# Performance work log

Measured on AMD Instinct MI355X. Metric: run time of the kernel, lower is better.

The kernel has to match this reference:

```python
import jax, jax.numpy as jnp
import numpy as np


def setup_inputs() -> dict:
    key = jax.random.key(0)
    ks = jax.random.split(key, 9)
    B, C, H, W = 1, 128, 96, 96
    Ci = C // 2
    s = 1.0 / np.sqrt(C)
    return {
        "x": jax.random.normal(ks[0], (B, C, H, W), dtype=jnp.float32),
        "theta_w": jax.random.normal(ks[1], (Ci, C), dtype=jnp.float32) * s,
        "theta_b": jax.random.normal(ks[2], (Ci,), dtype=jnp.float32) * 0.01,
        "phi_w": jax.random.normal(ks[3], (Ci, C), dtype=jnp.float32) * s,
        "phi_b": jax.random.normal(ks[4], (Ci,), dtype=jnp.float32) * 0.01,
        "g_w": jax.random.normal(ks[5], (Ci, C), dtype=jnp.float32) * s,
        "g_b": jax.random.normal(ks[6], (Ci,), dtype=jnp.float32) * 0.01,
        "out_w": jax.random.normal(ks[7], (C, Ci), dtype=jnp.float32) * (1.0 / np.sqrt(Ci)),
        "out_b": jax.random.normal(ks[8], (C,), dtype=jnp.float32) * 0.01,
    }


def reference(x, theta_w, theta_b, phi_w, phi_b, g_w, g_b, out_w, out_b):
    B, C, H, W = x.shape
    # 1x1 convs == per-position linear projections; flatten spatial to N tokens
    xf = x.transpose(0, 2, 3, 1).reshape(-1, C)          # (N, C), N = B*H*W
    theta = xf @ theta_w.T + theta_b                     # (N, Ci)
    phi = xf @ phi_w.T + phi_b                           # (N, Ci)
    g = xf @ g_w.T + g_b                                 # (N, Ci)
    # unscaled non-local attention with double softmax
    attn = jax.nn.softmax(theta @ phi.T, axis=-1)        # (N, N)
    y = jax.nn.softmax(attn @ g, axis=-1)                # (N, Ci)
    out = y @ out_w.T + out_b                            # (N, C)
    return out.reshape(B, H, W, C).transpose(0, 3, 1, 2) + x
```

## Files before the change

### kernel.cpp

```cpp
#include <hip/hip_runtime.h>
#include <hip/hip_bf16.h>

#define N_TOK 9216
#define C_IN  128
#define CI    64
#define SPLITS 8
#define L2E   1.44269504088896340736f

typedef __bf16 bf16x8 __attribute__((ext_vector_type(8)));
typedef unsigned short u16;
typedef u16 u16x4 __attribute__((ext_vector_type(4)));
typedef u16 u16x8 __attribute__((ext_vector_type(8)));
typedef unsigned u32x4 __attribute__((ext_vector_type(4)));
typedef float f32x4 __attribute__((ext_vector_type(4)));

static __device__ __forceinline__ u16 f2bf(float f) {
  return __builtin_bit_cast(u16, __float2bfloat16(f));
}
static __device__ __forceinline__ float bf2f(u16 b) {
  unsigned u = ((unsigned)b) << 16;
  return __builtin_bit_cast(float, u);
}
static __device__ __forceinline__ bf16x8 pack8(const float* f) {
  u16x8 t;
#pragma unroll
  for (int j = 0; j < 8; ++j) t[j] = f2bf(f[j]);
  return __builtin_bit_cast(bf16x8, t);
}
static __device__ __forceinline__ bf16x8 load_bf8(const u16* p) {
  u32x4 v = *(const u32x4*)p;
  return __builtin_bit_cast(bf16x8, v);
}
static __device__ __forceinline__ void gload_lds16(const void* g, void* l) {
  __builtin_amdgcn_global_load_lds(
      (const __attribute__((address_space(1))) void*)g,
      (__attribute__((address_space(3))) void*)l, 16, 0, 0);
}

#define MFMA16(a, b, c) __builtin_amdgcn_mfma_f32_16x16x32_bf16((a), (b), (c), 0, 0, 0)

__global__ __launch_bounds__(256) void k1_proj(
    const float* __restrict__ x,
    const float* __restrict__ tw, const float* __restrict__ tb,
    const float* __restrict__ pw, const float* __restrict__ pb,
    const float* __restrict__ gw, const float* __restrict__ gb,
    u16* __restrict__ thetaF, u16* __restrict__ phiF, u16* __restrict__ vF)
{
  __shared__ u16 sbuf[64 * 72];
  const int tid = threadIdx.x;
  const int w = tid >> 6, lane = tid & 63;
  const int lr = lane & 15, lg = lane >> 4;
  const int p0 = blockIdx.x * 64;
  const int m = blockIdx.y;

  bf16x8 bf[4][4];
#pragma unroll
  for (int nt = 0; nt < 4; ++nt) {
    const int p = p0 + nt * 16 + lr;
#pragma unroll
    for (int kc = 0; kc < 4; ++kc) {
      const int c0 = kc * 32 + lg * 8;
      float f[8];
#pragma unroll
      for (int j = 0; j < 8; ++j) f[j] = x[(c0 + j) * N_TOK + p];
      bf[nt][kc] = pack8(f);
    }
  }

  const float* Wm = (m == 0) ? tw : (m == 1) ? pw : gw;
  const float* Bm = (m == 0) ? tb : (m == 1) ? pb : gb;

  bf16x8 af[4];
#pragma unroll
  for (int kc = 0; kc < 4; ++kc) {
    const float* src = Wm + (w * 16 + lr) * C_IN + kc * 32 + lg * 8;
    float f[8];
#pragma unroll
    for (int j = 0; j < 8; ++j) f[j] = src[j];
    af[kc] = pack8(f);
  }
  f32x4 acc[4];
#pragma unroll
  for (int nt = 0; nt < 4; ++nt) acc[nt] = f32x4{0.f, 0.f, 0.f, 0.f};
#pragma unroll
  for (int kc = 0; kc < 4; ++kc)
#pragma unroll
    for (int nt = 0; nt < 4; ++nt)
      acc[nt] = MFMA16(af[kc], bf[nt][kc], acc[nt]);

  float bias[4];
#pragma unroll
  for (int r = 0; r < 4; ++r) bias[r] = Bm[w * 16 + lg * 4 + r];

  const float oscale = (m == 0) ? L2E : 1.0f;

  if (m < 2) {
#pragma unroll
    for (int nt = 0; nt < 4; ++nt)
#pragma unroll
      for (int r = 0; r < 4; ++r)
        sbuf[(nt * 16 + lr) * 72 + (w * 16 + lg * 4 + r)] =
            f2bf((acc[nt][r] + bias[r]) * oscale);
    __syncthreads();
    if (m == 0) {
#pragma unroll
      for (int e = 0; e < 2; ++e) {
        const int ch = tid * 2 + e;
        const int ln = ch & 63, c = (ch >> 6) & 1, qt = ch >> 7;
        const int ql = qt * 16 + (ln & 15), d = c * 32 + (ln >> 4) * 8;
        u32x4 v = *(const u32x4*)&sbuf[ql * 72 + d];
        *(u32x4*)&thetaF[(((size_t)(p0 / 16 + qt) * 2 + c) * 64 + ln) * 8] = v;
      }
    } else {
#pragma unroll
      for (int e = 0; e < 2; ++e) {
        const int ch = tid * 2 + e;
        const int ln = ch & 63, i = (ch >> 6) & 3, t = ch >> 8;
        const int kl = t * 32 + (i >> 1) * 16 + (ln & 15);
        const int d = (i & 1) * 32 + (ln >> 4) * 8;
        u32x4 v = *(const u32x4*)&sbuf[kl * 72 + d];
        *(u32x4*)&phiF[(((size_t)(p0 / 32 + t) * 4 + i) * 64 + ln) * 8] = v;
      }
    }
  } else {
#pragma unroll
    for (int nt = 0; nt < 4; ++nt)
#pragma unroll
      for (int r = 0; r < 4; ++r)
        sbuf[(w * 16 + lg * 4 + r) * 72 + nt * 16 + lr] = f2bf(acc[nt][r] + bias[r]);
    __syncthreads();
#pragma unroll
    for (int e = 0; e < 2; ++e) {
      const int ch = tid * 2 + e;
      const int ln = ch & 63, n = (ch >> 6) & 3, t = ch >> 8;
      const int d = n * 16 + (ln & 15), g4 = (ln >> 4) * 4;
      u16x4 lo = *(const u16x4*)&sbuf[d * 72 + t * 32 + g4];
      u16x4 hi = *(const u16x4*)&sbuf[d * 72 + t * 32 + 16 + g4];
      u16x8 v;
#pragma unroll
      for (int j = 0; j < 4; ++j) { v[j] = lo[j]; v[4 + j] = hi[j]; }
      *(u16x8*)&vF[(((size_t)(p0 / 32 + t) * 4 + n) * 64 + ln) * 8] = v;
    }
  }
}

__global__ __launch_bounds__(256) void k2_flash(
    const u16* __restrict__ thetaF, const u16* __restrict__ phiF,
    const u16* __restrict__ vF,
    u16* __restrict__ Opart, float* __restrict__ Lpart)
{
  __shared__ u16 kvbuf[2][8][512];
  const int tid = threadIdx.x;
  const int w = tid >> 6, lane = tid & 63;
  const int lr = lane & 15, g = lane >> 4;
  const int ks = blockIdx.x & 7;
  const int qt = blockIdx.x >> 3;
  const int q0 = qt * 128 + w * 32;
  const int NT64 = (N_TOK / SPLITS) / 64;
  const int t64base = ks * NT64;

  bf16x8 qb[2][2];
#pragma unroll
  for (int qs = 0; qs < 2; ++qs)
#pragma unroll
    for (int c = 0; c < 2; ++c)
      qb[qs][c] = load_bf8(&thetaF[(((size_t)(q0 / 16 + qs) * 2 + c) * 64 + lane) * 8]);

  f32x4 o[2][4], o4[2];
#pragma unroll
  for (int qs = 0; qs < 2; ++qs) {
#pragma unroll
    for (int n = 0; n < 4; ++n) o[qs][n] = f32x4{0.f, 0.f, 0.f, 0.f};
    o4[qs] = f32x4{0.f, 0.f, 0.f, 0.f};
  }

  u16x8 onesw;
#pragma unroll
  for (int j = 0; j < 8; ++j) onesw[j] = 0x3F80;
  const bf16x8 ones = __builtin_bit_cast(bf16x8, onesw);

  const int f0 = 2 * w;
  const size_t kgoff = (size_t)(f0 & 3) * 512 + lane * 8;
  const int hW = w >> 1;

#define STAGE(T, buf)                                                         \
  {                                                                           \
    const u16* gp = phiF + (size_t)(2 * (t64base + (T)) + hW) * 2048 + kgoff; \
    gload_lds16(gp, &kvbuf[buf][f0][0]);                                      \
    gload_lds16(gp + 512, &kvbuf[buf][f0 + 1][0]);                            \
  }

  STAGE(0, 0);
  __syncthreads();

  int cur = 0;
  for (int T = 0; T < NT64; ++T) {
    bf16x8 va[2][4];
    const u16* pV = vF + (size_t)(2 * (t64base + T)) * 2048 + lane * 8;
#pragma unroll
    for (int h = 0; h < 2; ++h)
#pragma unroll
      for (int n = 0; n < 4; ++n)
        va[h][n] = load_bf8(pV + (size_t)(h * 4 + n) * 512);

    if (T + 1 < NT64) STAGE(T + 1, cur ^ 1);

#pragma unroll
    for (int h = 0; h < 2; ++h) {
      const bf16x8 ka0 = load_bf8(&kvbuf[cur][h * 4 + 0][lane * 8]);
      const bf16x8 ka1 = load_bf8(&kvbuf[cur][h * 4 + 1][lane * 8]);
      const bf16x8 ka2 = load_bf8(&kvbuf[cur][h * 4 + 2][lane * 8]);
      const bf16x8 ka3 = load_bf8(&kvbuf[cur][h * 4 + 3][lane * 8]);

#pragma unroll
      for (int qs = 0; qs < 2; ++qs) {
        f32x4 s0 = f32x4{0.f, 0.f, 0.f, 0.f}, s1 = f32x4{0.f, 0.f, 0.f, 0.f};
        s0 = MFMA16(ka0, qb[qs][0], s0); s0 = MFMA16(ka1, qb[qs][1], s0);
        s1 = MFMA16(ka2, qb[qs][0], s1); s1 = MFMA16(ka3, qb[qs][1], s1);

        float p0v[4], p1v[4];
#pragma unroll
        for (int r = 0; r < 4; ++r) {
          p0v[r] = __builtin_amdgcn_exp2f(s0[r]);
          p1v[r] = __builtin_amdgcn_exp2f(s1[r]);
        }
        u16x8 pw;
#pragma unroll
        for (int r = 0; r < 4; ++r) { pw[r] = f2bf(p0v[r]); pw[4 + r] = f2bf(p1v[r]); }
        const bf16x8 pb = __builtin_bit_cast(bf16x8, pw);
#pragma unroll
        for (int n = 0; n < 4; ++n) o[qs][n] = MFMA16(va[h][n], pb, o[qs][n]);
        o4[qs] = MFMA16(ones, pb, o4[qs]);
      }
    }

    __syncthreads();
    cur ^= 1;
  }

  const int qg = ks * N_TOK + q0;
#pragma unroll
  for (int qs = 0; qs < 2; ++qs) {
#pragma unroll
    for (int n = 0; n < 4; ++n) {
      u16x4 ov;
#pragma unroll
      for (int r = 0; r < 4; ++r) ov[r] = f2bf(o[qs][n][r]);
      *(u16x4*)&Opart[(size_t)(qg + qs * 16 + lr) * CI + n * 16 + 4 * g] = ov;
    }
    if (lane < 16) Lpart[qg + qs * 16 + lr] = o4[qs][0];
  }
}

__global__ __launch_bounds__(256) void k2b_combine(
    const u16* __restrict__ Opart, const float* __restrict__ Lpart,
    u16* __restrict__ y)
{
  const int tid = threadIdx.x;
  const int w = tid >> 6, lane = tid & 63;
  const int q = blockIdx.x * 4 + w;

  float L = 0.f, acc = 0.f;
#pragma unroll
  for (int k = 0; k < SPLITS; ++k) {
    L += Lpart[k * N_TOK + q];
    acc += bf2f(Opart[(size_t)(k * N_TOK + q) * CI + lane]);
  }
  const float ypre = acc / L;

  float mx = ypre;
#pragma unroll
  for (int off = 1; off <= 32; off <<= 1) mx = fmaxf(mx, __shfl_xor(mx, off, 64));
  const float e = __builtin_amdgcn_exp2f((ypre - mx) * L2E);
  float s = e;
#pragma unroll
  for (int off = 1; off <= 32; off <<= 1) s += __shfl_xor(s, off, 64);
  y[q * CI + lane] = f2bf(e / s);
}

__global__ __launch_bounds__(256) void k3_out(
    const u16* __restrict__ y, const float* __restrict__ ow,
    const float* __restrict__ ob, const float* __restrict__ x,
    float* __restrict__ out)
{
  const int tid = threadIdx.x;
  const int w = tid >> 6, lane = tid & 63;
  const int lr = lane & 15, lg = lane >> 4;
  const int p0 = blockIdx.x * 32;

  bf16x8 yb[2][2];
#pragma unroll
  for (int nt = 0; nt < 2; ++nt)
#pragma unroll
    for (int kc = 0; kc < 2; ++kc)
      yb[nt][kc] = load_bf8(&y[(p0 + nt * 16 + lr) * CI + kc * 32 + lg * 8]);

#pragma unroll
  for (int mt = 0; mt < 2; ++mt) {
    bf16x8 af[2];
#pragma unroll
    for (int kc = 0; kc < 2; ++kc) {
      const float* src = ow + (w * 32 + mt * 16 + lr) * CI + kc * 32 + lg * 8;
      float f[8];
#pragma unroll
      for (int j = 0; j < 8; ++j) f[j] = src[j];
      af[kc] = pack8(f);
    }
#pragma unroll
    for (int nt = 0; nt < 2; ++nt) {
      f32x4 acc = f32x4{0.f, 0.f, 0.f, 0.f};
      acc = MFMA16(af[0], yb[nt][0], acc);
      acc = MFMA16(af[1], yb[nt][1], acc);
#pragma unroll
      for (int r = 0; r < 4; ++r) {
        const int c = w * 32 + mt * 16 + lg * 4 + r;
        const int p = p0 + nt * 16 + lr;
        out[(size_t)c * N_TOK + p] = acc[r] + ob[c] + x[(size_t)c * N_TOK + p];
      }
    }
  }
}

extern "C" void kernel_launch(void* const* d_in, const int* in_sizes, int n_in,
                              void* d_out, int out_size, void* d_ws, size_t ws_size,
                              hipStream_t stream) {
  const float* x  = (const float*)d_in[0];
  const float* tw = (const float*)d_in[1];
  const float* tb = (const float*)d_in[2];
  const float* pw = (const float*)d_in[3];
  const float* pb = (const float*)d_in[4];
  const float* gw = (const float*)d_in[5];
  const float* gb = (const float*)d_in[6];
  const float* ow = (const float*)d_in[7];
  const float* ob = (const float*)d_in[8];
  float* out = (float*)d_out;

  char* ws = (char*)d_ws;
  u16* thetaF = (u16*)(ws);
  u16* phiF   = (u16*)(ws + 1179648);
  u16* vF     = (u16*)(ws + 2 * 1179648);
  u16* yb     = (u16*)(ws + 3 * 1179648);
  u16* Op     = (u16*)(ws + 4 * 1179648);
  float* Lp   = (float*)(ws + 4 * 1179648 + 9437184);

  hipLaunchKernelGGL(k1_proj, dim3(144, 3), dim3(256), 0, stream,
                     x, tw, tb, pw, pb, gw, gb, thetaF, phiF, vF);
  hipLaunchKernelGGL(k2_flash, dim3(72 * SPLITS), dim3(256), 0, stream,
                     thetaF, phiF, vF, Op, Lp);
  hipLaunchKernelGGL(k2b_combine, dim3(N_TOK / 4), dim3(256), 0, stream,
                     Op, Lp, yb);
  hipLaunchKernelGGL(k3_out, dim3(288), dim3(256), 0, stream,
                     yb, ow, ob, x, out);
}
```

Baseline: 61.59 us.

## Stage V tiles through LDS and raise flash split count to 16

The flash kernel now stages both phi and V tiles into a double-buffered LDS buffer. All four waves issue async global-to-LDS copies, replacing the per-wave direct global loads of V, so each V tile is fetched once per block instead of once per wave. The split-K count goes from 8 to 16 when the workspace is large enough, which doubles the number of blocks for better CU occupancy. The cost is twice as many partial outputs for the combine kernel to read and reduce, plus doubled LDS use per block.

```diff
diff --git a/kernel.cpp b/kernel.cpp
--- a/kernel.cpp
+++ b/kernel.cpp
@@ -4,7 +4,6 @@
 #define N_TOK 9216
 #define C_IN  128
 #define CI    64
-#define SPLITS 8
 #define L2E   1.44269504088896340736f
 
 typedef __bf16 bf16x8 __attribute__((ext_vector_type(8)));
@@ -144,19 +143,20 @@
   }
 }
 
+template <int SPL>
 __global__ __launch_bounds__(256) void k2_flash(
     const u16* __restrict__ thetaF, const u16* __restrict__ phiF,
     const u16* __restrict__ vF,
     u16* __restrict__ Opart, float* __restrict__ Lpart)
 {
-  __shared__ u16 kvbuf[2][8][512];
+  __shared__ u16 kvbuf[2][16][512];
   const int tid = threadIdx.x;
   const int w = tid >> 6, lane = tid & 63;
   const int lr = lane & 15, g = lane >> 4;
-  const int ks = blockIdx.x & 7;
-  const int qt = blockIdx.x >> 3;
+  const int ks = blockIdx.x & (SPL - 1);
+  const int qt = blockIdx.x / SPL;
   const int q0 = qt * 128 + w * 32;
-  const int NT64 = (N_TOK / SPLITS) / 64;
+  const int NT64 = (N_TOK / SPL) / 64;
   const int t64base = ks * NT64;
 
   bf16x8 qb[2][2];
@@ -179,15 +179,18 @@
   for (int j = 0; j < 8; ++j) onesw[j] = 0x3F80;
   const bf16x8 ones = __builtin_bit_cast(bf16x8, onesw);
 
-  const int f0 = 2 * w;
-  const size_t kgoff = (size_t)(f0 & 3) * 512 + lane * 8;
-  const int hW = w >> 1;
-
-#define STAGE(T, buf)                                                         \
-  {                                                                           \
-    const u16* gp = phiF + (size_t)(2 * (t64base + (T)) + hW) * 2048 + kgoff; \
-    gload_lds16(gp, &kvbuf[buf][f0][0]);                                      \
-    gload_lds16(gp + 512, &kvbuf[buf][f0 + 1][0]);                            \
+  const u16* sbase = (w < 2) ? phiF : vF;
+  const int fbase = w * 4;
+  const int sub = w & 1;
+
+#define STAGE(T, buf)                                                          \
+  {                                                                            \
+    const u16* gp = sbase + (size_t)(2 * (t64base + (T)) + sub) * 2048 +       \
+                    lane * 8;                                                  \
+    gload_lds16(gp,        &kvbuf[buf][fbase][0]);                             \
+    gload_lds16(gp + 512,  &kvbuf[buf][fbase + 1][0]);                         \
+    gload_lds16(gp + 1024, &kvbuf[buf][fbase + 2][0]);                         \
+    gload_lds16(gp + 1536, &kvbuf[buf][fbase + 3][0]);                         \
   }
 
   STAGE(0, 0);
@@ -195,14 +198,6 @@
 
   int cur = 0;
   for (int T = 0; T < NT64; ++T) {
-    bf16x8 va[2][4];
-    const u16* pV = vF + (size_t)(2 * (t64base + T)) * 2048 + lane * 8;
-#pragma unroll
-    for (int h = 0; h < 2; ++h)
-#pragma unroll
-      for (int n = 0; n < 4; ++n)
-        va[h][n] = load_bf8(pV + (size_t)(h * 4 + n) * 512);
-
     if (T + 1 < NT64) STAGE(T + 1, cur ^ 1);
 
 #pragma unroll
@@ -211,6 +206,9 @@
       const bf16x8 ka1 = load_bf8(&kvbuf[cur][h * 4 + 1][lane * 8]);
       const bf16x8 ka2 = load_bf8(&kvbuf[cur][h * 4 + 2][lane * 8]);
       const bf16x8 ka3 = load_bf8(&kvbuf[cur][h * 4 + 3][lane * 8]);
+      bf16x8 va[4];
+#pragma unroll
+      for (int n = 0; n < 4; ++n) va[n] = load_bf8(&kvbuf[cur][8 + h * 4 + n][lane * 8]);
 
 #pragma unroll
       for (int qs = 0; qs < 2; ++qs) {
@@ -229,7 +227,7 @@
         for (int r = 0; r < 4; ++r) { pw[r] = f2bf(p0v[r]); pw[4 + r] = f2bf(p1v[r]); }
         const bf16x8 pb = __builtin_bit_cast(bf16x8, pw);
 #pragma unroll
-        for (int n = 0; n < 4; ++n) o[qs][n] = MFMA16(va[h][n], pb, o[qs][n]);
+        for (int n = 0; n < 4; ++n) o[qs][n] = MFMA16(va[n], pb, o[qs][n]);
         o4[qs] = MFMA16(ones, pb, o4[qs]);
       }
     }
@@ -252,6 +250,7 @@
   }
 }
 
+template <int SPL>
 __global__ __launch_bounds__(256) void k2b_combine(
     const u16* __restrict__ Opart, const float* __restrict__ Lpart,
     u16* __restrict__ y)
@@ -262,7 +261,7 @@
 
   float L = 0.f, acc = 0.f;
 #pragma unroll
-  for (int k = 0; k < SPLITS; ++k) {
+  for (int k = 0; k < SPL; ++k) {
     L += Lpart[k * N_TOK + q];
     acc += bf2f(Opart[(size_t)(k * N_TOK + q) * CI + lane]);
   }
@@ -341,14 +340,27 @@
   u16* vF     = (u16*)(ws + 2 * 1179648);
   u16* yb     = (u16*)(ws + 3 * 1179648);
   u16* Op     = (u16*)(ws + 4 * 1179648);
-  float* Lp   = (float*)(ws + 4 * 1179648 + 9437184);
+
+  const size_t opOff = 4 * 1179648;
+  const size_t need16 = opOff + (size_t)16 * N_TOK * CI * 2 + (size_t)16 * N_TOK * 4;
 
   hipLaunchKernelGGL(k1_proj, dim3(144, 3), dim3(256), 0, stream,
                      x, tw, tb, pw, pb, gw, gb, thetaF, phiF, vF);
-  hipLaunchKernelGGL(k2_flash, dim3(72 * SPLITS), dim3(256), 0, stream,
-                     thetaF, phiF, vF, Op, Lp);
-  hipLaunchKernelGGL(k2b_combine, dim3(N_TOK / 4), dim3(256), 0, stream,
-                     Op, Lp, yb);
+
+  if (ws_size >= need16) {
+    float* Lp = (float*)(ws + opOff + (size_t)16 * N_TOK * CI * 2);
+    hipLaunchKernelGGL((k2_flash<16>), dim3(72 * 16), dim3(256), 0, stream,
+                       thetaF, phiF, vF, Op, Lp);
+    hipLaunchKernelGGL((k2b_combine<16>), dim3(N_TOK / 4), dim3(256), 0, stream,
+                       Op, Lp, yb);
+  } else {
+    float* Lp = (float*)(ws + opOff + (size_t)8 * N_TOK * CI * 2);
+    hipLaunchKernelGGL((k2_flash<8>), dim3(72 * 8), dim3(256), 0, stream,
+                       thetaF, phiF, vF, Op, Lp);
+    hipLaunchKernelGGL((k2b_combine<8>), dim3(N_TOK / 4), dim3(256), 0, stream,
+                       Op, Lp, yb);
+  }
+
   hipLaunchKernelGGL(k3_out, dim3(288), dim3(256), 0, stream,
                      yb, ow, ob, x, out);
 }
```

Measured after the change: 59.06 us. -4.1%, faster.
